# Kernel optimization log

Measured on AMD Instinct MI355X. Metric: run time of the kernel, lower is better.

Reference implementation:

```python
import jax, jax.numpy as jnp
import numpy as np

B, T, C, H, D, G, V, M = 4, 1024, 768, 12, 4, 4, 32000, 1024
S = C // H


def layernorm(x, g, b, eps=1e-5):
    mu = jnp.mean(x, -1, keepdims=True)
    var = jnp.mean(jnp.square(x - mu), -1, keepdims=True)
    return (x - mu) * jax.lax.rsqrt(var + eps) * g + b


def setup_inputs() -> dict:
    key = jax.random.key(0)
    ks = jax.random.split(key, 12)
    std = 0.02  # matches _init_weights normal(0, 0.02)
    n = lambda k, sh: jax.random.normal(k, sh, jnp.float32) * std
    return {
        'x': jax.random.randint(ks[0], (B, T), 0, V),
        'y': jax.random.randint(ks[1], (B, T), 0, V),
        'wordemb': n(ks[2], (V, C)),
        'posemb': n(ks[3], (M, C)),
        'Wq': n(ks[4], (D, C, C)),
        'Wk': n(ks[5], (D, C, C)),
        'Wv': n(ks[6], (D, C, C)),
        'Wo': n(ks[7], (D, C, C)),
        'bo': jnp.zeros((D, C), jnp.float32),
        'ln1_g': jnp.ones((D, C), jnp.float32),
        'ln1_b': jnp.zeros((D, C), jnp.float32),
        'W1': n(ks[8], (D, C, G * C)),
        'b1': jnp.zeros((D, G * C), jnp.float32),
        'W2': n(ks[9], (D, G * C, C)),
        'b2': jnp.zeros((D, C), jnp.float32),
        'ln2_g': jnp.ones((D, C), jnp.float32),
        'ln2_b': jnp.zeros((D, C), jnp.float32),
        'Wl': n(ks[10], (C, V)),
        'bl': jnp.zeros((V,), jnp.float32),
    }


def _forward(x, y, wordemb, posemb, Wq, Wk, Wv, Wo, bo, ln1_g, ln1_b,
             W1, b1, W2, b2, ln2_g, ln2_b, Wl, bl):
    b, t = x.shape
    emb = wordemb[x] + posemb[:t][None, :, :]  # (b,t,c)
    causal = jnp.tril(jnp.ones((t, t), bool))

    def block(h_in, p):
        wq, wk, wv, wo, bo_, g1, be1, w1, b1_, w2, b2_, g2, be2 = p
        q = (h_in @ wq).reshape(b, t, H, S)
        k = (h_in @ wk).reshape(b, t, H, S)
        v = (h_in @ wv).reshape(b, t, H, S)
        # note: original scales by sqrt(channels), NOT sqrt(head_dim)
        w = jnp.einsum('bqhs,bkhs->bhqk', q, k) / jnp.sqrt(jnp.float32(C))
        w = jnp.where(causal, w, -jnp.inf)
        w = jax.nn.softmax(w, axis=-1)
        att = jnp.einsum('bhqk,bkhs->bqhs', w, v).reshape(b, t, C)
        att = att @ wo + bo_
        h1 = h_in + layernorm(att, g1, be1)   # x + norm1(attn(x))
        ff = jax.nn.relu(h1 @ w1 + b1_) @ w2 + b2_
        h2 = h1 + layernorm(ff, g2, be2)      # x + norm2(ff(x)); dropout=0
        return h2, None

    hfin, _ = jax.lax.scan(
        block, emb,
        (Wq, Wk, Wv, Wo, bo, ln1_g, ln1_b, W1, b1, W2, b2, ln2_g, ln2_b))
    logits = hfin @ Wl + bl  # (b,t,v)
    logp = jax.nn.log_softmax(logits, axis=-1)
    nll = -jnp.take_along_axis(logp, y[..., None], axis=-1)[..., 0]
    loss = jnp.mean(nll)
    return logits, loss


def reference(x, y, wordemb, posemb, Wq, Wk, Wv, Wo, bo, ln1_g, ln1_b,
              W1, b1, W2, b2, ln2_g, ln2_b, Wl, bl):
    return _forward(x, y, wordemb, posemb, Wq, Wk, Wv, Wo, bo, ln1_g, ln1_b,
                    W1, b1, W2, b2, ln2_g, ln2_b, Wl, bl)
```

## Files before the change

kernel.cpp:

```cpp
#include <hip/hip_runtime.h>

#define Bn 4
#define Tn 1024
#define Cn 768
#define Hn 12
#define Dn 4
#define Vn 32000
#define BTn (Bn*Tn)
#define NBX 125

typedef __attribute__((ext_vector_type(8))) short short8;
typedef __attribute__((ext_vector_type(4))) float f32x4;

__device__ __forceinline__ unsigned short f2bf(float f) {
  union { float f; unsigned u; } v; v.f = f;
  unsigned r = v.u + 0x7fffu + ((v.u >> 16) & 1u);
  return (unsigned short)(r >> 16);
}

__device__ __forceinline__ void gload_lds16(const void* g, void* l) {
  __builtin_amdgcn_global_load_lds(
      (const __attribute__((address_space(1))) void*)g,
      (__attribute__((address_space(3))) void*)l, 16, 0, 0);
}

__global__ __launch_bounds__(256)
void transpose_bf16_kernel(const float* __restrict__ src0, unsigned short* __restrict__ dst0,
                           int K, int N, size_t sStride, size_t dStride) {
  const float* src = src0 + blockIdx.z * sStride;
  unsigned short* dst = dst0 + blockIdx.z * dStride;
  __shared__ float tile[32][33];
  const int tx = threadIdx.x, ty = threadIdx.y;
  const int n0 = blockIdx.x * 32, k0 = blockIdx.y * 32;
#pragma unroll
  for (int i = 0; i < 4; ++i)
    tile[ty + i*8][tx] = src[(size_t)(k0 + ty + i*8) * N + n0 + tx];
  __syncthreads();
#pragma unroll
  for (int i = 0; i < 4; ++i)
    dst[(size_t)(n0 + ty + i*8) * K + k0 + tx] = f2bf(tile[tx][ty + i*8]);
}

__global__ __launch_bounds__(256)
void embed_kernel(const int* __restrict__ x, const float* __restrict__ wordemb,
                  const float* __restrict__ posemb, float* __restrict__ h,
                  unsigned short* __restrict__ hb) {
  int i4 = blockIdx.x * 256 + threadIdx.x;
  int row = i4 / (Cn/4), c4 = i4 % (Cn/4);
  int t = row & (Tn - 1);
  int tok = x[row];
  float4 a = ((const float4*)wordemb)[(size_t)tok * (Cn/4) + c4];
  float4 p = ((const float4*)posemb)[(size_t)t * (Cn/4) + c4];
  float4 s; s.x = a.x+p.x; s.y = a.y+p.y; s.z = a.z+p.z; s.w = a.w+p.w;
  ((float4*)h)[i4] = s;
  ushort4 u; u.x = f2bf(s.x); u.y = f2bf(s.y); u.z = f2bf(s.z); u.w = f2bf(s.w);
  ((ushort4*)hb)[i4] = u;
}

__global__ __launch_bounds__(256, 2)
void gemm_l(const unsigned short* __restrict__ A, const unsigned short* __restrict__ Bt,
            const float* __restrict__ bias, float* __restrict__ Cf,
            unsigned short* __restrict__ Cb, int M, int N, int K, int relu,
            unsigned short* __restrict__ vTp) {
  __shared__ __align__(16) unsigned short lds[2*16384];
  const int tid = threadIdx.x;
  const int gx = gridDim.x;
  const int flat = blockIdx.x + gx*blockIdx.y;
  const int chq = (gx * gridDim.y) >> 3;
  const int swz = (flat & 7)*chq + (flat >> 3);
  const int by = swz % gx, bx = swz / gx;
  const int lane = tid & 63, w = tid >> 6;
  const int wr = w >> 1, wc = w & 1;
  const int lr = lane & 15, lq = lane >> 4;
  const int xm = (lr >> 1) & 3;
  const int sslot = (lane & 3) ^ ((lane >> 3) & 3);
  const int NT = K >> 6;

  f32x4 acc[4][4];
#pragma unroll
  for (int i = 0; i < 4; ++i)
#pragma unroll
    for (int j = 0; j < 4; ++j)
      acc[i][j] = (f32x4){0.f, 0.f, 0.f, 0.f};

  const unsigned short* aS = A  + (size_t)(by*128 + w*16 + (lane>>2))*K + sslot*8;
  const unsigned short* bS = Bt + (size_t)(bx*128 + w*16 + (lane>>2))*K + sslot*8;

  auto stA = [&](int t) {
    unsigned short* d = &lds[(t&1)*16384];
    const int k0 = t*64;
#pragma unroll
    for (int kh = 0; kh < 2; ++kh)
#pragma unroll
      for (int i = 0; i < 2; ++i)
        gload_lds16(aS + k0 + kh*32 + (size_t)i*64*K, d + kh*4096 + (i*64 + w*16)*32);
  };
  auto stB = [&](int t) {
    unsigned short* d = &lds[(t&1)*16384 + 8192];
    const int k0 = t*64;
#pragma unroll
    for (int kh = 0; kh < 2; ++kh)
#pragma unroll
      for (int i = 0; i < 2; ++i)
        gload_lds16(bS + k0 + kh*32 + (size_t)i*64*K, d + kh*4096 + (i*64 + w*16)*32);
  };
  auto rdA = [&](int t, int kh, short8* af) {
    const unsigned short* p = &lds[(t&1)*16384 + kh*4096];
#pragma unroll
    for (int mi = 0; mi < 4; ++mi)
      af[mi] = *(const short8*)&p[(wr*64 + mi*16 + lr)*32 + (lq ^ xm)*8];
  };
  auto rdB = [&](int t, int kh, short8* bf) {
    const unsigned short* p = &lds[(t&1)*16384 + 8192 + kh*4096];
#pragma unroll
    for (int nj = 0; nj < 4; ++nj)
      bf[nj] = *(const short8*)&p[(wc*64 + nj*16 + lr)*32 + (lq ^ xm)*8];
  };

  short8 af0[4], af1[4], bf0[4], bf1[4];
  stA(0); stB(0); stA(1);

  for (int t = 0; t < NT; ++t) {
    if (t + 1 < NT) { asm volatile("s_waitcnt vmcnt(4)" ::: "memory"); }
    else            { asm volatile("s_waitcnt vmcnt(0)" ::: "memory"); }
    __builtin_amdgcn_s_barrier();
    __builtin_amdgcn_sched_barrier(0);
    rdA(t, 0, af0); rdA(t, 1, af1); rdB(t, 0, bf0);
    if (t + 1 < NT) stB(t + 1);
    __builtin_amdgcn_s_barrier();
    __builtin_amdgcn_sched_barrier(0);
    __builtin_amdgcn_s_setprio(1);
#pragma unroll
    for (int i = 0; i < 4; ++i)
#pragma unroll
      for (int j = 0; j < 4; ++j)
        acc[i][j] = __builtin_amdgcn_mfma_f32_16x16x32_bf16(af0[i], bf0[j], acc[i][j], 0, 0, 0);
    __builtin_amdgcn_s_setprio(0);
    __builtin_amdgcn_s_barrier();
    rdB(t, 1, bf1);
    if (t + 2 < NT) stA(t + 2);
    __builtin_amdgcn_s_barrier();
    __builtin_amdgcn_sched_barrier(0);
    __builtin_amdgcn_s_setprio(1);
#pragma unroll
    for (int i = 0; i < 4; ++i)
#pragma unroll
      for (int j = 0; j < 4; ++j)
        acc[i][j] = __builtin_amdgcn_mfma_f32_16x16x32_bf16(af1[i], bf1[j], acc[i][j], 0, 0, 0);
    __builtin_amdgcn_s_setprio(0);
  }

  const bool isV = (vTp != nullptr) && (bx*128 >= 1536);
  if (!isV) {
#pragma unroll
    for (int mi = 0; mi < 4; ++mi)
#pragma unroll
      for (int nj = 0; nj < 4; ++nj)
#pragma unroll
        for (int r = 0; r < 4; ++r) {
          int grow = by*128 + wr*64 + mi*16 + lq*4 + r;
          int gcol = bx*128 + wc*64 + nj*16 + lr;
          float v = acc[mi][nj][r];
          if (bias) v += bias[gcol];
          if (relu) v = fmaxf(v, 0.f);
          size_t idx = (size_t)grow * N + gcol;
          if (Cf) Cf[idx] = v;
          if (Cb) Cb[idx] = f2bf(v);
        }
  } else {
    __syncthreads();
    unsigned short (*tile)[136] = (unsigned short (*)[136])lds;
#pragma unroll
    for (int mi = 0; mi < 4; ++mi)
#pragma unroll
      for (int nj = 0; nj < 4; ++nj)
#pragma unroll
        for (int r = 0; r < 4; ++r) {
          int lt = wr*64 + mi*16 + lq*4 + r;
          int ld = wc*64 + nj*16 + lr;
          tile[ld][lt] = f2bf(acc[mi][nj][r]);
        }
    __syncthreads();
    const int bq = (by*128) >> 10;
    const int t0 = (by*128) & 1023;
#pragma unroll
    for (int i = 0; i < 32; ++i) {
      int ld = w*32 + i;
      int gd = bx*128 + ld - 1536;
      int hh2 = gd >> 6, dd = gd & 63;
      ushort2 val = *(ushort2*)&tile[ld][2*lane];
      *(ushort2*)&vTp[((size_t)((bq*Hn + hh2)*64 + dd))*Tn + t0 + 2*lane] = val;
    }
  }
}

__global__ __launch_bounds__(512, 1)
void gemm_vocab(const unsigned short* __restrict__ A, const unsigned short* __restrict__ Bt,
                const float* __restrict__ bias, float* __restrict__ Cf,
                float2* __restrict__ lsepart) {
  constexpr int K = 768, N = Vn, NT = 12;
  __shared__ __align__(16) unsigned short lds[2*32768];
  const int tid = threadIdx.x;
  const int bid = blockIdx.x;
  const int swz = (bid & 7)*250 + (bid >> 3);
  const int by = swz & 15, bx = swz >> 4;
  const int lane = tid & 63, w = tid >> 6;
  const int wr = w >> 2, wc = w & 3;
  const int lr = lane & 15, lq = lane >> 4;
  const int xm = (lr >> 1) & 3;
  const int sslot = (lane & 3) ^ ((lane >> 3) & 3);

  f32x4 accLo[4][4], accHi[4][4];
#pragma unroll
  for (int i = 0; i < 4; ++i)
#pragma unroll
    for (int j = 0; j < 4; ++j) {
      accLo[i][j] = (f32x4){0.f,0.f,0.f,0.f};
      accHi[i][j] = (f32x4){0.f,0.f,0.f,0.f};
    }

  const unsigned short* aS = A  + (size_t)(by*256 + w*16 + (lane>>2))*K + sslot*8;
  const unsigned short* bS = Bt + (size_t)(bx*256 + w*16 + (lane>>2))*K + sslot*8;

  auto stA = [&](int t) {
    unsigned short* d = &lds[(t&1)*32768];
    const int k0 = t*64;
#pragma unroll
    for (int kh = 0; kh < 2; ++kh)
#pragma unroll
      for (int i = 0; i < 2; ++i)
        gload_lds16(aS + k0 + kh*32 + (size_t)i*128*K, d + kh*8192 + (i*128 + w*16)*32);
  };
  auto stB = [&](int t) {
    unsigned short* d = &lds[(t&1)*32768 + 16384];
    const int k0 = t*64;
#pragma unroll
    for (int kh = 0; kh < 2; ++kh)
#pragma unroll
      for (int i = 0; i < 2; ++i)
        gload_lds16(bS + k0 + kh*32 + (size_t)i*128*K, d + kh*8192 + (i*128 + w*16)*32);
  };
  auto rdA = [&](int t, int kh, int mh, short8* af) {
    const unsigned short* p = &lds[(t&1)*32768 + kh*8192];
#pragma unroll
    for (int mi = 0; mi < 4; ++mi)
      af[mi] = *(const short8*)&p[(wr*128 + mh*64 + mi*16 + lr)*32 + (lq ^ xm)*8];
  };
  auto rdB = [&](int t, int kh, short8* bf) {
    const unsigned short* p = &lds[(t&1)*32768 + 16384 + kh*8192];
#pragma unroll
    for (int nj = 0; nj < 4; ++nj)
      bf[nj] = *(const short8*)&p[(wc*64 + nj*16 + lr)*32 + (lq ^ xm)*8];
  };

  short8 aLo0[4], aHi0[4], aLo1[4], aHi1[4], bf0[4], bf1[4];
  stA(0); stB(0); stA(1); stB(1);

  for (int t = 0; t < NT; ++t) {
    if (t + 1 < NT) { asm volatile("s_waitcnt vmcnt(8)" ::: "memory"); }
    else            { asm volatile("s_waitcnt vmcnt(0)" ::: "memory"); }
    __builtin_amdgcn_s_barrier();
    __builtin_amdgcn_sched_barrier(0);
    rdA(t, 0, 0, aLo0); rdA(t, 0, 1, aHi0); rdB(t, 0, bf0);
    __builtin_amdgcn_s_barrier();
    __builtin_amdgcn_sched_barrier(0);
    __builtin_amdgcn_s_setprio(1);
#pragma unroll
    for (int i = 0; i < 4; ++i)
#pragma unroll
      for (int j = 0; j < 4; ++j)
        accLo[i][j] = __builtin_amdgcn_mfma_f32_16x16x32_bf16(aLo0[i], bf0[j], accLo[i][j], 0, 0, 0);
    __builtin_amdgcn_s_setprio(0);
    __builtin_amdgcn_s_barrier();
    rdA(t, 1, 0, aLo1); rdA(t, 1, 1, aHi1);
    __builtin_amdgcn_s_barrier();
    __builtin_amdgcn_sched_barrier(0);
    __builtin_amdgcn_s_setprio(1);
#pragma unroll
    for (int i = 0; i < 4; ++i)
#pragma unroll
      for (int j = 0; j < 4; ++j)
        accHi[i][j] = __builtin_amdgcn_mfma_f32_16x16x32_bf16(aHi0[i], bf0[j], accHi[i][j], 0, 0, 0);
    __builtin_amdgcn_s_setprio(0);
    __builtin_amdgcn_s_barrier();
    rdB(t, 1, bf1);
    if (t + 2 < NT) stA(t + 2);
    __builtin_amdgcn_s_barrier();
    __builtin_amdgcn_sched_barrier(0);
    __builtin_amdgcn_s_setprio(1);
#pragma unroll
    for (int i = 0; i < 4; ++i)
#pragma unroll
      for (int j = 0; j < 4; ++j)
        accLo[i][j] = __builtin_amdgcn_mfma_f32_16x16x32_bf16(aLo1[i], bf1[j], accLo[i][j], 0, 0, 0);
    __builtin_amdgcn_s_setprio(0);
    __builtin_amdgcn_s_barrier();
    if (t + 2 < NT) stB(t + 2);
    __builtin_amdgcn_s_barrier();
    __builtin_amdgcn_sched_barrier(0);
    __builtin_amdgcn_s_setprio(1);
#pragma unroll
    for (int i = 0; i < 4; ++i)
#pragma unroll
      for (int j = 0; j < 4; ++j)
        accHi[i][j] = __builtin_amdgcn_mfma_f32_16x16x32_bf16(aHi1[i], bf1[j], accHi[i][j], 0, 0, 0);
    __builtin_amdgcn_s_setprio(0);
  }

  float2* part = (float2*)lds;
#pragma unroll
  for (int half = 0; half < 2; ++half) {
#pragma unroll
    for (int mi = 0; mi < 4; ++mi)
#pragma unroll
      for (int r = 0; r < 4; ++r) {
        float v[4]; float m = -3.0e38f;
#pragma unroll
        for (int nj = 0; nj < 4; ++nj) {
          int gcol = bx*256 + wc*64 + nj*16 + lr;
          float val = (half ? accHi[mi][nj][r] : accLo[mi][nj][r]) + bias[gcol];
          v[nj] = val;
          m = fmaxf(m, val);
        }
        int prow = wr*128 + half*64 + mi*16 + lq*4 + r;
        int grow = by*256 + prow;
        float* crow = Cf + (size_t)grow * N + bx*256 + wc*64 + lr;
#pragma unroll
        for (int nj = 0; nj < 4; ++nj) crow[nj*16] = v[nj];
        float s = 0.f;
#pragma unroll
        for (int nj = 0; nj < 4; ++nj) s += __expf(v[nj] - m);
#pragma unroll
        for (int mask = 1; mask < 16; mask <<= 1) {
          float m2 = __shfl_xor(m, mask), s2 = __shfl_xor(s, mask);
          float mn = fmaxf(m, m2);
          s = s*__expf(m - mn) + s2*__expf(m2 - mn);
          m = mn;
        }
        if (lr == 0) part[prow*4 + wc] = make_float2(m, s);
      }
  }
  __syncthreads();
  if (tid < 256) {
    float2 p = part[tid*4];
    float m = p.x, s = p.y;
#pragma unroll
    for (int wcc = 1; wcc < 4; ++wcc) {
      float2 p2 = part[tid*4 + wcc];
      float mn = fmaxf(m, p2.x);
      s = s*__expf(m - mn) + p2.y*__expf(p2.x - mn);
      m = mn;
    }
    lsepart[(size_t)(by*256 + tid)*NBX + bx] = make_float2(m, s);
  }
}

__global__ __launch_bounds__(256)
void attn_mfma_kernel(const unsigned short* __restrict__ qkvb,
                      const unsigned short* __restrict__ vT,
                      unsigned short* __restrict__ attb) {
  const int qb = blockIdx.x, hh = blockIdx.y, b = blockIdx.z;
  const int t = threadIdx.x;
  const int lane = t & 63, w = t >> 6;
  const int lr = lane & 15, lg = lane >> 4;
  const float scale = 0.03608439182435161f;

  __shared__ unsigned short Ks[2][64*64];
  __shared__ unsigned short Vs[2][64*64];
  __shared__ unsigned short Ps[4][16][72];

  const unsigned short* qsrc = qkvb + (size_t)(b*Tn + qb*64 + w*16 + lr)*2304 + hh*64 + lg*8;
  short8 qa0 = *(const short8*)(qsrc);
  short8 qa1 = *(const short8*)(qsrc + 32);

  f32x4 acc[4];
#pragma unroll
  for (int dt = 0; dt < 4; ++dt) acc[dt] = (f32x4){0.f,0.f,0.f,0.f};
  float m_run[4], l_run[4];
#pragma unroll
  for (int r = 0; r < 4; ++r) { m_run[r] = -1e30f; l_run[r] = 0.f; }

  const int sr = t >> 2, c2 = t & 3;

  auto stage = [&](int kvb) {
    const int buf = kvb & 1;
    const unsigned short* ksrc = qkvb + (size_t)(b*Tn + kvb*64 + sr)*2304 + 768 + hh*64 + c2*16;
    short8 k0 = *(const short8*)ksrc;
    short8 k1 = *(const short8*)(ksrc + 8);
    const unsigned short* vsrc = vT + ((size_t)((b*Hn + hh)*64 + sr))*Tn + kvb*64 + c2*16;
    short8 vv0 = *(const short8*)vsrc;
    short8 vv1 = *(const short8*)(vsrc + 8);
    int s0 = (2*c2) ^ (sr & 7), s1 = (2*c2 + 1) ^ (sr & 7);
    *(short8*)&Ks[buf][sr*64 + s0*8] = k0;
    *(short8*)&Ks[buf][sr*64 + s1*8] = k1;
    *(short8*)&Vs[buf][sr*64 + s0*8] = vv0;
    *(short8*)&Vs[buf][sr*64 + s1*8] = vv1;
  };

  stage(0);
  __syncthreads();

  for (int kvb = 0; kvb <= qb; ++kvb) {
    if (kvb < qb) stage(kvb + 1);
    const int buf = kvb & 1;

    f32x4 s[4];
#pragma unroll
    for (int kt = 0; kt < 4; ++kt) {
      int krow = kt*16 + lr;
      short8 kf0 = *(const short8*)&Ks[buf][krow*64 + ((0 + lg) ^ (krow & 7))*8];
      short8 kf1 = *(const short8*)&Ks[buf][krow*64 + ((4 + lg) ^ (krow & 7))*8];
      f32x4 a = (f32x4){0.f,0.f,0.f,0.f};
      a = __builtin_amdgcn_mfma_f32_16x16x32_bf16(qa0, kf0, a, 0, 0, 0);
      a = __builtin_amdgcn_mfma_f32_16x16x32_bf16(qa1, kf1, a, 0, 0, 0);
      s[kt] = a;
    }
    const bool diag = (kvb == qb);
#pragma unroll
    for (int kt = 0; kt < 4; ++kt)
#pragma unroll
      for (int r = 0; r < 4; ++r) {
        float v = s[kt][r] * scale;
        if (diag && (kt*16 + lr > w*16 + lg*4 + r)) v = -1e30f;
        s[kt][r] = v;
      }
#pragma unroll
    for (int r = 0; r < 4; ++r) {
      float m = fmaxf(fmaxf(s[0][r], s[1][r]), fmaxf(s[2][r], s[3][r]));
      m = fmaxf(m, __shfl_xor(m, 1));
      m = fmaxf(m, __shfl_xor(m, 2));
      m = fmaxf(m, __shfl_xor(m, 4));
      m = fmaxf(m, __shfl_xor(m, 8));
      float mn = fmaxf(m_run[r], m);
      float corr = __expf(m_run[r] - mn);
      m_run[r] = mn;
      float ps = 0.f;
#pragma unroll
      for (int kt = 0; kt < 4; ++kt) {
        float p = __expf(s[kt][r] - mn);
        s[kt][r] = p;
        ps += p;
      }
      ps += __shfl_xor(ps, 1);
      ps += __shfl_xor(ps, 2);
      ps += __shfl_xor(ps, 4);
      ps += __shfl_xor(ps, 8);
      l_run[r] = l_run[r] * corr + ps;
#pragma unroll
      for (int dt = 0; dt < 4; ++dt) acc[dt][r] *= corr;
    }
#pragma unroll
    for (int kt = 0; kt < 4; ++kt)
#pragma unroll
      for (int r = 0; r < 4; ++r)
        Ps[w][lg*4 + r][kt*16 + lr] = f2bf(s[kt][r]);
    short8 pa0 = *(const short8*)&Ps[w][lr][lg*8];
    short8 pa1 = *(const short8*)&Ps[w][lr][32 + lg*8];
#pragma unroll
    for (int dt = 0; dt < 4; ++dt) {
      int drow = dt*16 + lr;
      short8 vf0 = *(const short8*)&Vs[buf][drow*64 + ((0 + lg) ^ (drow & 7))*8];
      short8 vf1 = *(const short8*)&Vs[buf][drow*64 + ((4 + lg) ^ (drow & 7))*8];
      acc[dt] = __builtin_amdgcn_mfma_f32_16x16x32_bf16(pa0, vf0, acc[dt], 0, 0, 0);
      acc[dt] = __builtin_amdgcn_mfma_f32_16x16x32_bf16(pa1, vf1, acc[dt], 0, 0, 0);
    }
    __syncthreads();
  }

  unsigned short* obase = attb + (size_t)(b*Tn + qb*64 + w*16)*768 + hh*64;
#pragma unroll
  for (int dt = 0; dt < 4; ++dt)
#pragma unroll
    for (int r = 0; r < 4; ++r) {
      float v = acc[dt][r] / l_run[r];
      obase[(size_t)(lg*4 + r)*768 + dt*16 + lr] = f2bf(v);
    }
}

__global__ __launch_bounds__(256)
void ln_res_kernel(const float* __restrict__ x, float* __restrict__ h,
                   unsigned short* __restrict__ hb, const float* __restrict__ g,
                   const float* __restrict__ bb) {
  const int lane = threadIdx.x & 63;
  const int row = blockIdx.x*4 + (threadIdx.x >> 6);
  const float4* xr4 = (const float4*)(x + (size_t)row * Cn);
  float4 v[3];
  float s1 = 0.f, s2 = 0.f;
#pragma unroll
  for (int j = 0; j < 3; ++j) {
    v[j] = xr4[lane + j*64];
    s1 += v[j].x + v[j].y + v[j].z + v[j].w;
    s2 += v[j].x*v[j].x + v[j].y*v[j].y + v[j].z*v[j].z + v[j].w*v[j].w;
  }
#pragma unroll
  for (int m = 1; m < 64; m <<= 1) { s1 += __shfl_xor(s1, m); s2 += __shfl_xor(s2, m); }
  float mu = s1 * (1.f/768.f);
  float var = s2 * (1.f/768.f) - mu*mu;
  float rs = rsqrtf(var + 1e-5f);
  float4* hr4 = (float4*)(h + (size_t)row * Cn);
  ushort4* hb4 = (ushort4*)(hb + (size_t)row * Cn);
  const float4* g4 = (const float4*)g;
  const float4* b4 = (const float4*)bb;
#pragma unroll
  for (int j = 0; j < 3; ++j) {
    int c = lane + j*64;
    float4 hv = hr4[c], gv = g4[c], bv = b4[c];
    float4 y;
    y.x = hv.x + (v[j].x - mu)*rs*gv.x + bv.x;
    y.y = hv.y + (v[j].y - mu)*rs*gv.y + bv.y;
    y.z = hv.z + (v[j].z - mu)*rs*gv.z + bv.z;
    y.w = hv.w + (v[j].w - mu)*rs*gv.w + bv.w;
    hr4[c] = y;
    ushort4 u; u.x = f2bf(y.x); u.y = f2bf(y.y); u.z = f2bf(y.z); u.w = f2bf(y.w);
    hb4[c] = u;
  }
}

__global__ __launch_bounds__(128)
void loss_part_kernel(const float2* __restrict__ part, const float* __restrict__ logits,
                      const int* __restrict__ y, float* __restrict__ loss_rows) {
  const int row = blockIdx.x, tid = threadIdx.x;
  float m = -3.0e38f, s = 0.f;
  if (tid < NBX) { float2 p = part[(size_t)row*NBX + tid]; m = p.x; s = p.y; }
#pragma unroll
  for (int mask = 1; mask < 64; mask <<= 1) {
    float m2 = __shfl_xor(m, mask), s2 = __shfl_xor(s, mask);
    float mn = fmaxf(m, m2);
    s = s*__expf(m - mn) + s2*__expf(m2 - mn);
    m = mn;
  }
  __shared__ float mw[2], sw[2];
  if ((tid & 63) == 0) { mw[tid >> 6] = m; sw[tid >> 6] = s; }
  __syncthreads();
  if (tid == 0) {
    float m2 = mw[1], s2 = sw[1];
    float mn = fmaxf(m, m2);
    s = s*__expf(m - mn) + s2*__expf(m2 - mn);
    loss_rows[row] = mn + __logf(s) - logits[(size_t)row*Vn + y[row]];
  }
}

__global__ __launch_bounds__(256)
void loss_reduce_kernel(const float* __restrict__ loss_rows, float* __restrict__ out) {
  const int tid = threadIdx.x;
  float s = 0.f;
  for (int j = 0; j < BTn/256; ++j) s += loss_rows[tid + j*256];
  __shared__ float red[256];
  red[tid] = s; __syncthreads();
  for (int st = 128; st > 0; st >>= 1) {
    if (tid < st) red[tid] += red[tid+st];
    __syncthreads();
  }
  if (tid == 0) out[0] = red[0] * (1.f/(float)BTn);
}

extern "C" void kernel_launch(void* const* d_in, const int* in_sizes, int n_in,
                              void* d_out, int out_size, void* d_ws, size_t ws_size,
                              hipStream_t stream) {
  const int*   x       = (const int*)  d_in[0];
  const int*   y       = (const int*)  d_in[1];
  const float* wordemb = (const float*)d_in[2];
  const float* posemb  = (const float*)d_in[3];
  const float* Wq      = (const float*)d_in[4];
  const float* Wk      = (const float*)d_in[5];
  const float* Wv      = (const float*)d_in[6];
  const float* Wo      = (const float*)d_in[7];
  const float* bo      = (const float*)d_in[8];
  const float* ln1_g   = (const float*)d_in[9];
  const float* ln1_b   = (const float*)d_in[10];
  const float* W1      = (const float*)d_in[11];
  const float* b1      = (const float*)d_in[12];
  const float* W2      = (const float*)d_in[13];
  const float* b2      = (const float*)d_in[14];
  const float* ln2_g   = (const float*)d_in[15];
  const float* ln2_b   = (const float*)d_in[16];
  const float* Wl      = (const float*)d_in[17];
  const float* bl      = (const float*)d_in[18];

  char* ws = (char*)d_ws;
  size_t off = 0;
  auto alloc = [&](size_t bytes) -> char* {
    char* p = ws + off;
    off += (bytes + 255) & ~(size_t)255;
    return p;
  };
  unsigned short* wqkvT = (unsigned short*)alloc((size_t)Dn*2304*768*2);
  unsigned short* woT   = (unsigned short*)alloc((size_t)Dn*768*768*2);
  unsigned short* w1T   = (unsigned short*)alloc((size_t)Dn*3072*768*2);
  unsigned short* w2T   = (unsigned short*)alloc((size_t)Dn*768*3072*2);
  unsigned short* wlT   = (unsigned short*)alloc((size_t)Vn*768*2);
  float*          h     = (float*)alloc((size_t)BTn*Cn*4);
  unsigned short* hb    = (unsigned short*)alloc((size_t)BTn*Cn*2);
  unsigned short* qkvb  = (unsigned short*)alloc((size_t)BTn*3072*2);
  unsigned short* vTb   = (unsigned short*)alloc((size_t)Bn*Hn*64*Tn*2);
  unsigned short* attb  = (unsigned short*)alloc((size_t)BTn*Cn*2);
  float*          tmp   = (float*)alloc((size_t)BTn*Cn*4);
  float*          loss_rows = (float*)alloc((size_t)BTn*4);
  float2*         lsepart   = (float2*)alloc((size_t)BTn*NBX*8);
  unsigned short* ff1b  = qkvb;

  dim3 tb(32, 8);
  transpose_bf16_kernel<<<dim3(24,24,Dn), tb, 0, stream>>>(Wq, wqkvT,             Cn, Cn, (size_t)Cn*Cn, (size_t)2304*768);
  transpose_bf16_kernel<<<dim3(24,24,Dn), tb, 0, stream>>>(Wk, wqkvT + 768*768,   Cn, Cn, (size_t)Cn*Cn, (size_t)2304*768);
  transpose_bf16_kernel<<<dim3(24,24,Dn), tb, 0, stream>>>(Wv, wqkvT + 1536*768,  Cn, Cn, (size_t)Cn*Cn, (size_t)2304*768);
  transpose_bf16_kernel<<<dim3(24,24,Dn), tb, 0, stream>>>(Wo, woT,               Cn, Cn, (size_t)Cn*Cn, (size_t)768*768);
  transpose_bf16_kernel<<<dim3(96,24,Dn), tb, 0, stream>>>(W1, w1T, 768, 3072, (size_t)768*3072, (size_t)3072*768);
  transpose_bf16_kernel<<<dim3(24,96,Dn), tb, 0, stream>>>(W2, w2T, 3072, 768, (size_t)3072*768, (size_t)768*3072);
  transpose_bf16_kernel<<<dim3(1000,24,1), tb, 0, stream>>>(Wl, wlT, 768, Vn, 0, 0);

  embed_kernel<<<(BTn*Cn/4)/256, 256, 0, stream>>>(x, wordemb, posemb, h, hb);

  for (int d = 0; d < Dn; ++d) {
    gemm_l<<<dim3(BTn/128, 2304/128), 256, 0, stream>>>(
        hb, wqkvT + (size_t)d*2304*768, nullptr, nullptr, qkvb, BTn, 2304, 768, 0, vTb);
    attn_mfma_kernel<<<dim3(Tn/64, Hn, Bn), 256, 0, stream>>>(qkvb, vTb, attb);
    gemm_l<<<dim3(BTn/128, 768/128), 256, 0, stream>>>(
        attb, woT + (size_t)d*768*768, bo + (size_t)d*768, tmp, nullptr, BTn, 768, 768, 0, nullptr);
    ln_res_kernel<<<BTn/4, 256, 0, stream>>>(tmp, h, hb, ln1_g + (size_t)d*768, ln1_b + (size_t)d*768);
    gemm_l<<<dim3(BTn/128, 3072/128), 256, 0, stream>>>(
        hb, w1T + (size_t)d*3072*768, b1 + (size_t)d*3072, nullptr, ff1b, BTn, 3072, 768, 1, nullptr);
    gemm_l<<<dim3(BTn/128, 768/128), 256, 0, stream>>>(
        ff1b, w2T + (size_t)d*768*3072, b2 + (size_t)d*768, tmp, nullptr, BTn, 768, 3072, 0, nullptr);
    ln_res_kernel<<<BTn/4, 256, 0, stream>>>(tmp, h, hb, ln2_g + (size_t)d*768, ln2_b + (size_t)d*768);
  }

  float* logits = (float*)d_out;
  gemm_vocab<<<2000, 512, 0, stream>>>(hb, wlT, bl, logits, lsepart);
  loss_part_kernel<<<BTn, 128, 0, stream>>>(lsepart, logits, y, loss_rows);
  loss_reduce_kernel<<<1, 256, 0, stream>>>(loss_rows, logits + (size_t)BTn*Vn);
}
```

Baseline: 1.304 ms.

## Shrink vocab GEMM tiles to 128x128 and double attention query block

The vocab projection GEMM drops from 256x256 tiles with 512 threads to 128x128 tiles with 256 threads, allowing two blocks per CU. It uses a 2D grid with a chunked swizzle and a simpler two-stage load schedule, and doubles the LSE partial count to match. The attention kernel now processes 128 query rows per 512-thread block, with K and V staging split across thread halves and per-warp diagonal skipping. The intent is better occupancy and load balance, at the cost of less operand reuse per tile in the GEMM and some idle warps in attention on off-diagonal tiles.

```diff
diff --git a/kernel.cpp b/kernel.cpp
--- a/kernel.cpp
+++ b/kernel.cpp
@@ -7,7 +7,7 @@
 #define Dn 4
 #define Vn 32000
 #define BTn (Bn*Tn)
-#define NBX 125
+#define NBX 250
 
 typedef __attribute__((ext_vector_type(8))) short short8;
 typedef __attribute__((ext_vector_type(4))) float f32x4;
@@ -194,74 +194,75 @@
   }
 }
 
-__global__ __launch_bounds__(512, 1)
+__global__ __launch_bounds__(256, 2)
 void gemm_vocab(const unsigned short* __restrict__ A, const unsigned short* __restrict__ Bt,
                 const float* __restrict__ bias, float* __restrict__ Cf,
                 float2* __restrict__ lsepart) {
   constexpr int K = 768, N = Vn, NT = 12;
-  __shared__ __align__(16) unsigned short lds[2*32768];
+  __shared__ __align__(16) unsigned short lds[2*16384];
   const int tid = threadIdx.x;
-  const int bid = blockIdx.x;
-  const int swz = (bid & 7)*250 + (bid >> 3);
-  const int by = swz & 15, bx = swz >> 4;
+  const int gx = gridDim.x;
+  const int flat = blockIdx.x + gx*blockIdx.y;
+  const int chq = (gx * gridDim.y) >> 3;
+  const int swz = (flat & 7)*chq + (flat >> 3);
+  const int by = swz % gx, bx = swz / gx;
   const int lane = tid & 63, w = tid >> 6;
-  const int wr = w >> 2, wc = w & 3;
+  const int wr = w >> 1, wc = w & 1;
   const int lr = lane & 15, lq = lane >> 4;
   const int xm = (lr >> 1) & 3;
   const int sslot = (lane & 3) ^ ((lane >> 3) & 3);
 
-  f32x4 accLo[4][4], accHi[4][4];
+  f32x4 acc[4][4];
 #pragma unroll
   for (int i = 0; i < 4; ++i)
 #pragma unroll
-    for (int j = 0; j < 4; ++j) {
-      accLo[i][j] = (f32x4){0.f,0.f,0.f,0.f};
-      accHi[i][j] = (f32x4){0.f,0.f,0.f,0.f};
-    }
-
-  const unsigned short* aS = A  + (size_t)(by*256 + w*16 + (lane>>2))*K + sslot*8;
-  const unsigned short* bS = Bt + (size_t)(bx*256 + w*16 + (lane>>2))*K + sslot*8;
+    for (int j = 0; j < 4; ++j)
+      acc[i][j] = (f32x4){0.f, 0.f, 0.f, 0.f};
+
+  const unsigned short* aS = A  + (size_t)(by*128 + w*16 + (lane>>2))*K + sslot*8;
+  const unsigned short* bS = Bt + (size_t)(bx*128 + w*16 + (lane>>2))*K + sslot*8;
 
   auto stA = [&](int t) {
-    unsigned short* d = &lds[(t&1)*32768];
+    unsigned short* d = &lds[(t&1)*16384];
     const int k0 = t*64;
 #pragma unroll
     for (int kh = 0; kh < 2; ++kh)
 #pragma unroll
       for (int i = 0; i < 2; ++i)
-        gload_lds16(aS + k0 + kh*32 + (size_t)i*128*K, d + kh*8192 + (i*128 + w*16)*32);
+        gload_lds16(aS + k0 + kh*32 + (size_t)i*64*K, d + kh*4096 + (i*64 + w*16)*32);
   };
   auto stB = [&](int t) {
-    unsigned short* d = &lds[(t&1)*32768 + 16384];
+    unsigned short* d = &lds[(t&1)*16384 + 8192];
     const int k0 = t*64;
 #pragma unroll
     for (int kh = 0; kh < 2; ++kh)
 #pragma unroll
       for (int i = 0; i < 2; ++i)
-        gload_lds16(bS + k0 + kh*32 + (size_t)i*128*K, d + kh*8192 + (i*128 + w*16)*32);
-  };
-  auto rdA = [&](int t, int kh, int mh, short8* af) {
-    const unsigned short* p = &lds[(t&1)*32768 + kh*8192];
+        gload_lds16(bS + k0 + kh*32 + (size_t)i*64*K, d + kh*4096 + (i*64 + w*16)*32);
+  };
+  auto rdA = [&](int t, int kh, short8* af) {
+    const unsigned short* p = &lds[(t&1)*16384 + kh*4096];
 #pragma unroll
     for (int mi = 0; mi < 4; ++mi)
-      af[mi] = *(const short8*)&p[(wr*128 + mh*64 + mi*16 + lr)*32 + (lq ^ xm)*8];
+      af[mi] = *(const short8*)&p[(wr*64 + mi*16 + lr)*32 + (lq ^ xm)*8];
   };
   auto rdB = [&](int t, int kh, short8* bf) {
-    const unsigned short* p = &lds[(t&1)*32768 + 16384 + kh*8192];
+    const unsigned short* p = &lds[(t&1)*16384 + 8192 + kh*4096];
 #pragma unroll
     for (int nj = 0; nj < 4; ++nj)
       bf[nj] = *(const short8*)&p[(wc*64 + nj*16 + lr)*32 + (lq ^ xm)*8];
   };
 
-  short8 aLo0[4], aHi0[4], aLo1[4], aHi1[4], bf0[4], bf1[4];
-  stA(0); stB(0); stA(1); stB(1);
+  short8 af0[4], af1[4], bf0[4], bf1[4];
+  stA(0); stB(0); stA(1);
 
   for (int t = 0; t < NT; ++t) {
-    if (t + 1 < NT) { asm volatile("s_waitcnt vmcnt(8)" ::: "memory"); }
+    if (t + 1 < NT) { asm volatile("s_waitcnt vmcnt(4)" ::: "memory"); }
     else            { asm volatile("s_waitcnt vmcnt(0)" ::: "memory"); }
     __builtin_amdgcn_s_barrier();
     __builtin_amdgcn_sched_barrier(0);
-    rdA(t, 0, 0, aLo0); rdA(t, 0, 1, aHi0); rdB(t, 0, bf0);
+    rdA(t, 0, af0); rdA(t, 1, af1); rdB(t, 0, bf0);
+    if (t + 1 < NT) stB(t + 1);
     __builtin_amdgcn_s_barrier();
     __builtin_amdgcn_sched_barrier(0);
     __builtin_amdgcn_s_setprio(1);
@@ -269,10 +270,11 @@
     for (int i = 0; i < 4; ++i)
 #pragma unroll
       for (int j = 0; j < 4; ++j)
-        accLo[i][j] = __builtin_amdgcn_mfma_f32_16x16x32_bf16(aLo0[i], bf0[j], accLo[i][j], 0, 0, 0);
+        acc[i][j] = __builtin_amdgcn_mfma_f32_16x16x32_bf16(af0[i], bf0[j], acc[i][j], 0, 0, 0);
     __builtin_amdgcn_s_setprio(0);
     __builtin_amdgcn_s_barrier();
-    rdA(t, 1, 0, aLo1); rdA(t, 1, 1, aHi1);
+    rdB(t, 1, bf1);
+    if (t + 2 < NT) stA(t + 2);
     __builtin_amdgcn_s_barrier();
     __builtin_amdgcn_sched_barrier(0);
     __builtin_amdgcn_s_setprio(1);
@@ -280,82 +282,51 @@
     for (int i = 0; i < 4; ++i)
 #pragma unroll
       for (int j = 0; j < 4; ++j)
-        accHi[i][j] = __builtin_amdgcn_mfma_f32_16x16x32_bf16(aHi0[i], bf0[j], accHi[i][j], 0, 0, 0);
+        acc[i][j] = __builtin_amdgcn_mfma_f32_16x16x32_bf16(af1[i], bf1[j], acc[i][j], 0, 0, 0);
     __builtin_amdgcn_s_setprio(0);
-    __builtin_amdgcn_s_barrier();
-    rdB(t, 1, bf1);
-    if (t + 2 < NT) stA(t + 2);
-    __builtin_amdgcn_s_barrier();
-    __builtin_amdgcn_sched_barrier(0);
-    __builtin_amdgcn_s_setprio(1);
-#pragma unroll
-    for (int i = 0; i < 4; ++i)
-#pragma unroll
-      for (int j = 0; j < 4; ++j)
-        accLo[i][j] = __builtin_amdgcn_mfma_f32_16x16x32_bf16(aLo1[i], bf1[j], accLo[i][j], 0, 0, 0);
-    __builtin_amdgcn_s_setprio(0);
-    __builtin_amdgcn_s_barrier();
-    if (t + 2 < NT) stB(t + 2);
-    __builtin_amdgcn_s_barrier();
-    __builtin_amdgcn_sched_barrier(0);
-    __builtin_amdgcn_s_setprio(1);
-#pragma unroll
-    for (int i = 0; i < 4; ++i)
-#pragma unroll
-      for (int j = 0; j < 4; ++j)
-        accHi[i][j] = __builtin_amdgcn_mfma_f32_16x16x32_bf16(aHi1[i], bf1[j], accHi[i][j], 0, 0, 0);
-    __builtin_amdgcn_s_setprio(0);
-  }
-
+  }
+
+  __syncthreads();
   float2* part = (float2*)lds;
 #pragma unroll
-  for (int half = 0; half < 2; ++half) {
-#pragma unroll
-    for (int mi = 0; mi < 4; ++mi)
-#pragma unroll
-      for (int r = 0; r < 4; ++r) {
-        float v[4]; float m = -3.0e38f;
-#pragma unroll
-        for (int nj = 0; nj < 4; ++nj) {
-          int gcol = bx*256 + wc*64 + nj*16 + lr;
-          float val = (half ? accHi[mi][nj][r] : accLo[mi][nj][r]) + bias[gcol];
-          v[nj] = val;
-          m = fmaxf(m, val);
-        }
-        int prow = wr*128 + half*64 + mi*16 + lq*4 + r;
-        int grow = by*256 + prow;
-        float* crow = Cf + (size_t)grow * N + bx*256 + wc*64 + lr;
-#pragma unroll
-        for (int nj = 0; nj < 4; ++nj) crow[nj*16] = v[nj];
-        float s = 0.f;
-#pragma unroll
-        for (int nj = 0; nj < 4; ++nj) s += __expf(v[nj] - m);
-#pragma unroll
-        for (int mask = 1; mask < 16; mask <<= 1) {
-          float m2 = __shfl_xor(m, mask), s2 = __shfl_xor(s, mask);
-          float mn = fmaxf(m, m2);
-          s = s*__expf(m - mn) + s2*__expf(m2 - mn);
-          m = mn;
-        }
-        if (lr == 0) part[prow*4 + wc] = make_float2(m, s);
+  for (int mi = 0; mi < 4; ++mi)
+#pragma unroll
+    for (int r = 0; r < 4; ++r) {
+      float v[4]; float m = -3.0e38f;
+#pragma unroll
+      for (int nj = 0; nj < 4; ++nj) {
+        int gcol = bx*128 + wc*64 + nj*16 + lr;
+        float val = acc[mi][nj][r] + bias[gcol];
+        v[nj] = val;
+        m = fmaxf(m, val);
       }
-  }
+      int prow = wr*64 + mi*16 + lq*4 + r;
+      int grow = by*128 + prow;
+      float* crow = Cf + (size_t)grow * N + bx*128 + wc*64 + lr;
+#pragma unroll
+      for (int nj = 0; nj < 4; ++nj) crow[nj*16] = v[nj];
+      float s = 0.f;
+#pragma unroll
+      for (int nj = 0; nj < 4; ++nj) s += __expf(v[nj] - m);
+#pragma unroll
+      for (int mask = 1; mask < 16; mask <<= 1) {
+        float m2 = __shfl_xor(m, mask), s2 = __shfl_xor(s, mask);
+        float mn = fmaxf(m, m2);
+        s = s*__expf(m - mn) + s2*__expf(m2 - mn);
+        m = mn;
+      }
+      if (lr == 0) part[prow*2 + wc] = make_float2(m, s);
+    }
   __syncthreads();
-  if (tid < 256) {
-    float2 p = part[tid*4];
-    float m = p.x, s = p.y;
-#pragma unroll
-    for (int wcc = 1; wcc < 4; ++wcc) {
-      float2 p2 = part[tid*4 + wcc];
-      float mn = fmaxf(m, p2.x);
-      s = s*__expf(m - mn) + p2.y*__expf(p2.x - mn);
-      m = mn;
-    }
-    lsepart[(size_t)(by*256 + tid)*NBX + bx] = make_float2(m, s);
-  }
-}
-
-__global__ __launch_bounds__(256)
+  if (tid < 128) {
+    float2 p0 = part[tid*2], p1 = part[tid*2 + 1];
+    float mn = fmaxf(p0.x, p1.x);
+    float s = p0.y*__expf(p0.x - mn) + p1.y*__expf(p1.x - mn);
+    lsepart[(size_t)(by*128 + tid)*NBX + bx] = make_float2(mn, s);
+  }
+}
+
+__global__ __launch_bounds__(512)
 void attn_mfma_kernel(const unsigned short* __restrict__ qkvb,
                       const unsigned short* __restrict__ vT,
                       unsigned short* __restrict__ attb) {
@@ -367,9 +338,13 @@
 
   __shared__ unsigned short Ks[2][64*64];
   __shared__ unsigned short Vs[2][64*64];
-  __shared__ unsigned short Ps[4][16][72];
-
-  const unsigned short* qsrc = qkvb + (size_t)(b*Tn + qb*64 + w*16 + lr)*2304 + hh*64 + lg*8;
+  __shared__ unsigned short Ps[8][16][72];
+
+  const int R0 = qb*128 + w*16;
+  const int myDiag = R0 >> 6;
+  const int NTILES = 2*qb + 2;
+
+  const unsigned short* qsrc = qkvb + (size_t)(b*Tn + R0 + lr)*2304 + hh*64 + lg*8;
   short8 qa0 = *(const short8*)(qsrc);
   short8 qa1 = *(const short8*)(qsrc + 32);
 
@@ -380,94 +355,99 @@
 #pragma unroll
   for (int r = 0; r < 4; ++r) { m_run[r] = -1e30f; l_run[r] = 0.f; }
 
-  const int sr = t >> 2, c2 = t & 3;
+  const int sr = (t & 255) >> 2, c2 = t & 3;
 
   auto stage = [&](int kvb) {
     const int buf = kvb & 1;
-    const unsigned short* ksrc = qkvb + (size_t)(b*Tn + kvb*64 + sr)*2304 + 768 + hh*64 + c2*16;
-    short8 k0 = *(const short8*)ksrc;
-    short8 k1 = *(const short8*)(ksrc + 8);
-    const unsigned short* vsrc = vT + ((size_t)((b*Hn + hh)*64 + sr))*Tn + kvb*64 + c2*16;
-    short8 vv0 = *(const short8*)vsrc;
-    short8 vv1 = *(const short8*)(vsrc + 8);
     int s0 = (2*c2) ^ (sr & 7), s1 = (2*c2 + 1) ^ (sr & 7);
-    *(short8*)&Ks[buf][sr*64 + s0*8] = k0;
-    *(short8*)&Ks[buf][sr*64 + s1*8] = k1;
-    *(short8*)&Vs[buf][sr*64 + s0*8] = vv0;
-    *(short8*)&Vs[buf][sr*64 + s1*8] = vv1;
+    if (t < 256) {
+      const unsigned short* ksrc = qkvb + (size_t)(b*Tn + kvb*64 + sr)*2304 + 768 + hh*64 + c2*16;
+      short8 k0 = *(const short8*)ksrc;
+      short8 k1 = *(const short8*)(ksrc + 8);
+      *(short8*)&Ks[buf][sr*64 + s0*8] = k0;
+      *(short8*)&Ks[buf][sr*64 + s1*8] = k1;
+    } else {
+      const unsigned short* vsrc = vT + ((size_t)((b*Hn + hh)*64 + sr))*Tn + kvb*64 + c2*16;
+      short8 vv0 = *(const short8*)vsrc;
+      short8 vv1 = *(const short8*)(vsrc + 8);
+      *(short8*)&Vs[buf][sr*64 + s0*8] = vv0;
+      *(short8*)&Vs[buf][sr*64 + s1*8] = vv1;
+    }
   };
 
   stage(0);
   __syncthreads();
 
-  for (int kvb = 0; kvb <= qb; ++kvb) {
-    if (kvb < qb) stage(kvb + 1);
+  for (int kvb = 0; kvb < NTILES; ++kvb) {
+    if (kvb + 1 < NTILES) stage(kvb + 1);
     const int buf = kvb & 1;
 
-    f32x4 s[4];
-#pragma unroll
-    for (int kt = 0; kt < 4; ++kt) {
-      int krow = kt*16 + lr;
-      short8 kf0 = *(const short8*)&Ks[buf][krow*64 + ((0 + lg) ^ (krow & 7))*8];
-      short8 kf1 = *(const short8*)&Ks[buf][krow*64 + ((4 + lg) ^ (krow & 7))*8];
-      f32x4 a = (f32x4){0.f,0.f,0.f,0.f};
-      a = __builtin_amdgcn_mfma_f32_16x16x32_bf16(qa0, kf0, a, 0, 0, 0);
-      a = __builtin_amdgcn_mfma_f32_16x16x32_bf16(qa1, kf1, a, 0, 0, 0);
-      s[kt] = a;
-    }
-    const bool diag = (kvb == qb);
-#pragma unroll
-    for (int kt = 0; kt < 4; ++kt)
+    if (kvb <= myDiag) {
+      f32x4 s[4];
+#pragma unroll
+      for (int kt = 0; kt < 4; ++kt) {
+        int krow = kt*16 + lr;
+        short8 kf0 = *(const short8*)&Ks[buf][krow*64 + ((0 + lg) ^ (krow & 7))*8];
+        short8 kf1 = *(const short8*)&Ks[buf][krow*64 + ((4 + lg) ^ (krow & 7))*8];
+        f32x4 a = (f32x4){0.f,0.f,0.f,0.f};
+        a = __builtin_amdgcn_mfma_f32_16x16x32_bf16(qa0, kf0, a, 0, 0, 0);
+        a = __builtin_amdgcn_mfma_f32_16x16x32_bf16(qa1, kf1, a, 0, 0, 0);
+        s[kt] = a;
+      }
+      const bool diag = (kvb == myDiag);
+#pragma unroll
+      for (int kt = 0; kt < 4; ++kt)
+#pragma unroll
+        for (int r = 0; r < 4; ++r) {
+          float v = s[kt][r] * scale;
+          if (diag && (kt*16 + lr > (w & 3)*16 + lg*4 + r)) v = -1e30f;
+          s[kt][r] = v;
+        }
 #pragma unroll
       for (int r = 0; r < 4; ++r) {
-        float v = s[kt][r] * scale;
-        if (diag && (kt*16 + lr > w*16 + lg*4 + r)) v = -1e30f;
-        s[kt][r] = v;
+        float m = fmaxf(fmaxf(s[0][r], s[1][r]), fmaxf(s[2][r], s[3][r]));
+        m = fmaxf(m, __shfl_xor(m, 1));
+        m = fmaxf(m, __shfl_xor(m, 2));
+        m = fmaxf(m, __shfl_xor(m, 4));
+        m = fmaxf(m, __shfl_xor(m, 8));
+        float mn = fmaxf(m_run[r], m);
+        float corr = __expf(m_run[r] - mn);
+        m_run[r] = mn;
+        float ps = 0.f;
+#pragma unroll
+        for (int kt = 0; kt < 4; ++kt) {
+          float p = __expf(s[kt][r] - mn);
+          s[kt][r] = p;
+          ps += p;
+        }
+        ps += __shfl_xor(ps, 1);
+        ps += __shfl_xor(ps, 2);
+        ps += __shfl_xor(ps, 4);
+        ps += __shfl_xor(ps, 8);
+        l_run[r] = l_run[r] * corr + ps;
+#pragma unroll
+        for (int dt = 0; dt < 4; ++dt) acc[dt][r] *= corr;
       }
 #pragma unroll
-    for (int r = 0; r < 4; ++r) {
-      float m = fmaxf(fmaxf(s[0][r], s[1][r]), fmaxf(s[2][r], s[3][r]));
-      m = fmaxf(m, __shfl_xor(m, 1));
-      m = fmaxf(m, __shfl_xor(m, 2));
-      m = fmaxf(m, __shfl_xor(m, 4));
-      m = fmaxf(m, __shfl_xor(m, 8));
-      float mn = fmaxf(m_run[r], m);
-      float corr = __expf(m_run[r] - mn);
-      m_run[r] = mn;
-      float ps = 0.f;
-#pragma unroll
-      for (int kt = 0; kt < 4; ++kt) {
-        float p = __expf(s[kt][r] - mn);
-        s[kt][r] = p;
-        ps += p;
+      for (int kt = 0; kt < 4; ++kt)
+#pragma unroll
+        for (int r = 0; r < 4; ++r)
+          Ps[w][lg*4 + r][kt*16 + lr] = f2bf(s[kt][r]);
+      short8 pa0 = *(const short8*)&Ps[w][lr][lg*8];
+      short8 pa1 = *(const short8*)&Ps[w][lr][32 + lg*8];
+#pragma unroll
+      for (int dt = 0; dt < 4; ++dt) {
+        int drow = dt*16 + lr;
+        short8 vf0 = *(const short8*)&Vs[buf][drow*64 + ((0 + lg) ^ (drow & 7))*8];
+        short8 vf1 = *(const short8*)&Vs[buf][drow*64 + ((4 + lg) ^ (drow & 7))*8];
+        acc[dt] = __builtin_amdgcn_mfma_f32_16x16x32_bf16(pa0, vf0, acc[dt], 0, 0, 0);
+        acc[dt] = __builtin_amdgcn_mfma_f32_16x16x32_bf16(pa1, vf1, acc[dt], 0, 0, 0);
       }
-      ps += __shfl_xor(ps, 1);
-      ps += __shfl_xor(ps, 2);
-      ps += __shfl_xor(ps, 4);
-      ps += __shfl_xor(ps, 8);
-      l_run[r] = l_run[r] * corr + ps;
-#pragma unroll
-      for (int dt = 0; dt < 4; ++dt) acc[dt][r] *= corr;
-    }
-#pragma unroll
-    for (int kt = 0; kt < 4; ++kt)
-#pragma unroll
-      for (int r = 0; r < 4; ++r)
-        Ps[w][lg*4 + r][kt*16 + lr] = f2bf(s[kt][r]);
-    short8 pa0 = *(const short8*)&Ps[w][lr][lg*8];
-    short8 pa1 = *(const short8*)&Ps[w][lr][32 + lg*8];
-#pragma unroll
-    for (int dt = 0; dt < 4; ++dt) {
-      int drow = dt*16 + lr;
-      short8 vf0 = *(const short8*)&Vs[buf][drow*64 + ((0 + lg) ^ (drow & 7))*8];
-      short8 vf1 = *(const short8*)&Vs[buf][drow*64 + ((4 + lg) ^ (drow & 7))*8];
-      acc[dt] = __builtin_amdgcn_mfma_f32_16x16x32_bf16(pa0, vf0, acc[dt], 0, 0, 0);
-      acc[dt] = __builtin_amdgcn_mfma_f32_16x16x32_bf16(pa1, vf1, acc[dt], 0, 0, 0);
     }
     __syncthreads();
   }
 
-  unsigned short* obase = attb + (size_t)(b*Tn + qb*64 + w*16)*768 + hh*64;
+  unsigned short* obase = attb + (size_t)(b*Tn + R0)*768 + hh*64;
 #pragma unroll
   for (int dt = 0; dt < 4; ++dt)
 #pragma unroll
@@ -516,7 +496,7 @@
   }
 }
 
-__global__ __launch_bounds__(128)
+__global__ __launch_bounds__(256)
 void loss_part_kernel(const float2* __restrict__ part, const float* __restrict__ logits,
                       const int* __restrict__ y, float* __restrict__ loss_rows) {
   const int row = blockIdx.x, tid = threadIdx.x;
@@ -529,14 +509,17 @@
     s = s*__expf(m - mn) + s2*__expf(m2 - mn);
     m = mn;
   }
-  __shared__ float mw[2], sw[2];
+  __shared__ float mw[4], sw[4];
   if ((tid & 63) == 0) { mw[tid >> 6] = m; sw[tid >> 6] = s; }
   __syncthreads();
   if (tid == 0) {
-    float m2 = mw[1], s2 = sw[1];
-    float mn = fmaxf(m, m2);
-    s = s*__expf(m - mn) + s2*__expf(m2 - mn);
-    loss_rows[row] = mn + __logf(s) - logits[(size_t)row*Vn + y[row]];
+#pragma unroll
+    for (int i = 1; i < 4; ++i) {
+      float mn = fmaxf(m, mw[i]);
+      s = s*__expf(m - mn) + sw[i]*__expf(mw[i] - mn);
+      m = mn;
+    }
+    loss_rows[row] = m + __logf(s) - logits[(size_t)row*Vn + y[row]];
   }
 }
 
@@ -613,7 +596,7 @@
   for (int d = 0; d < Dn; ++d) {
     gemm_l<<<dim3(BTn/128, 2304/128), 256, 0, stream>>>(
         hb, wqkvT + (size_t)d*2304*768, nullptr, nullptr, qkvb, BTn, 2304, 768, 0, vTb);
-    attn_mfma_kernel<<<dim3(Tn/64, Hn, Bn), 256, 0, stream>>>(qkvb, vTb, attb);
+    attn_mfma_kernel<<<dim3(Tn/128, Hn, Bn), 512, 0, stream>>>(qkvb, vTb, attb);
     gemm_l<<<dim3(BTn/128, 768/128), 256, 0, stream>>>(
         attb, woT + (size_t)d*768*768, bo + (size_t)d*768, tmp, nullptr, BTn, 768, 768, 0, nullptr);
     ln_res_kernel<<<BTn/4, 256, 0, stream>>>(tmp, h, hb, ln1_g + (size_t)d*768, ln1_b + (size_t)d*768);
@@ -625,7 +608,7 @@
   }
 
   float* logits = (float*)d_out;
-  gemm_vocab<<<2000, 512, 0, stream>>>(hb, wlT, bl, logits, lsepart);
-  loss_part_kernel<<<BTn, 128, 0, stream>>>(lsepart, logits, y, loss_rows);
+  gemm_vocab<<<dim3(32, 250), 256, 0, stream>>>(hb, wlT, bl, logits, lsepart);
+  loss_part_kernel<<<BTn, 256, 0, stream>>>(lsepart, logits, y, loss_rows);
   loss_reduce_kernel<<<1, 256, 0, stream>>>(loss_rows, logits + (size_t)BTn*Vn);
 }
```

Result: slower. 1.483 ms (+13.8%).
